# Performance work log

Hardware: AMD Instinct MI355X
Metric: run time of the kernel (lower is better)

## Reference

```python
import jax, jax.numpy as jnp
import numpy as np

LL = 1 << 20            # Fastfood padded size (power of 2 >= DD)
DD = 1024 * 768         # out_features * in_features
OUT, IN = 1024, 768


def fwht(v):
    """Unnormalized fast Walsh-Hadamard transform over a length-2^k vector."""
    n = v.shape[0]
    h = 1
    while h < n:
        v = v.reshape(-1, 2, h)
        v = jnp.concatenate([v[:, 0] + v[:, 1], v[:, 0] - v[:, 1]], axis=-1)
        h *= 2
    return v.reshape(n)


def setup_inputs() -> dict:
    key = jax.random.key(0)
    ks = jax.random.split(key, 7)
    x = jax.random.normal(ks[0], (8, 2048, IN), dtype=jnp.float32)
    theta = jax.random.normal(ks[1], (2048,), dtype=jnp.float32)
    W_0 = jax.random.normal(ks[2], (OUT, IN), dtype=jnp.float32) * 0.02
    b = jax.random.normal(ks[3], (OUT,), dtype=jnp.float32) * 0.02
    # Rademacher +/-1 diagonal
    BB = (jax.random.bernoulli(ks[4], 0.5, (LL,)).astype(jnp.float32) * 2.0 - 1.0)
    GG = jax.random.normal(ks[5], (LL,), dtype=jnp.float32)
    Pi = jax.random.permutation(ks[6], LL).astype(jnp.int64)
    return {"x": x, "theta": theta, "W_0": W_0, "b": b, "BB": BB, "GG": GG, "Pi": Pi}


def reference(x, theta, W_0, b, BB, GG, Pi):
    # pad intrinsic parameter to LL (theta.numel() < LL branch)
    theta_pad = jnp.zeros((LL,), dtype=theta.dtype).at[: theta.shape[0]].set(theta)
    # Fastfood: H B theta -> permute -> G diag -> H
    v = fwht(BB * theta_pad)
    v = v[Pi] * GG
    v = fwht(v)
    divisor = jnp.sqrt(LL * jnp.sum(GG * GG))
    update_vec = v[:DD] / (divisor * np.sqrt(float(DD) / LL))
    W_eff = W_0 + update_vec.reshape(OUT, IN)
    return jnp.einsum("bsi,oi->bso", x, W_eff) + b
```

## Files before the change

kernel.cpp:

```cpp
#include <hip/hip_runtime.h>
#include <hip/hip_bf16.h>


#define LL (1 << 20)
#define DD (1024 * 768)
#define OUTF 1024
#define INF 768
#define MROWS 16384

typedef __attribute__((ext_vector_type(8))) short s16x8;
typedef __attribute__((ext_vector_type(4))) float f32x4;
typedef __attribute__((ext_vector_type(16))) float f32x16;

__device__ __forceinline__ unsigned short f2bf(float f) {
    union { float f; unsigned u; } v; v.f = f;
    unsigned r = v.u + 0x7FFF + ((v.u >> 16) & 1);
    return (unsigned short)(r >> 16);
}

__device__ __forceinline__ unsigned cvt_pk_bf16(float lo, float hi) {
    unsigned r;
    asm("v_cvt_pk_bf16_f32 %0, %1, %2" : "=v"(r) : "v"(lo), "v"(hi));
    return r;
}

__global__ void k01_cast_r01(const float* __restrict__ X, ushort* __restrict__ XB,
                             const float* __restrict__ BB, const float* __restrict__ theta,
                             float* __restrict__ r01g) {
    __shared__ float sx[2048];
    const int t = threadIdx.x;
    if (blockIdx.x < 2048) {
        const f32x4* X4 = (const f32x4*)X;
        s16x8* O = (s16x8*)XB;
        size_t i = (size_t)blockIdx.x * 256 + t;
        #pragma unroll
        for (int j = 0; j < 3; j++, i += 524288) {
            const f32x4 A = X4[2 * i];
            const f32x4 B = X4[2 * i + 1];
            union { s16x8 v; unsigned u[4]; } o;
            o.u[0] = cvt_pk_bf16(A.x, A.y);
            o.u[1] = cvt_pk_bf16(A.z, A.w);
            o.u[2] = cvt_pk_bf16(B.x, B.y);
            o.u[3] = cvt_pk_bf16(B.z, B.w);
            O[i] = o.v;
        }
        return;
    }
    const int r = t >> 7, tt = t & 127, lane = t & 63;
    float v[8];
    {
        const float4 a0 = *(const float4*)&BB[r * 1024 + tt * 8];
        const float4 a1 = *(const float4*)&BB[r * 1024 + tt * 8 + 4];
        const float4 b0 = *(const float4*)&theta[r * 1024 + tt * 8];
        const float4 b1 = *(const float4*)&theta[r * 1024 + tt * 8 + 4];
        v[0] = a0.x * b0.x; v[1] = a0.y * b0.y; v[2] = a0.z * b0.z; v[3] = a0.w * b0.w;
        v[4] = a1.x * b1.x; v[5] = a1.y * b1.y; v[6] = a1.z * b1.z; v[7] = a1.w * b1.w;
    }
    float a;
    a = v[0]; v[0] = a + v[1]; v[1] = a - v[1];
    a = v[2]; v[2] = a + v[3]; v[3] = a - v[3];
    a = v[4]; v[4] = a + v[5]; v[5] = a - v[5];
    a = v[6]; v[6] = a + v[7]; v[7] = a - v[7];
    a = v[0]; v[0] = a + v[2]; v[2] = a - v[2];
    a = v[1]; v[1] = a + v[3]; v[3] = a - v[3];
    a = v[4]; v[4] = a + v[6]; v[6] = a - v[6];
    a = v[5]; v[5] = a + v[7]; v[7] = a - v[7];
    a = v[0]; v[0] = a + v[4]; v[4] = a - v[4];
    a = v[1]; v[1] = a + v[5]; v[5] = a - v[5];
    a = v[2]; v[2] = a + v[6]; v[6] = a - v[6];
    a = v[3]; v[3] = a + v[7]; v[7] = a - v[7];
    #pragma unroll
    for (int j = 0; j < 6; j++) {
        const float sgn = ((lane >> j) & 1) ? -1.0f : 1.0f;
        #pragma unroll
        for (int c = 0; c < 8; c++) {
            float o = __shfl_xor(v[c], 1 << j, 64);
            v[c] = fmaf(sgn, v[c], o);
        }
    }
    #pragma unroll
    for (int c = 0; c < 8; c++) sx[r * 1024 + tt * 8 + c] = v[c];
    __syncthreads();
    {
        const int pt = r * 1024 + (tt ^ 64) * 8;
        const float sgn = (tt & 64) ? -1.0f : 1.0f;
        #pragma unroll
        for (int c = 0; c < 8; c++) v[c] = fmaf(sgn, v[c], sx[pt + c]);
    }
    #pragma unroll
    for (int c = 0; c < 8; c++) r01g[r * 1024 + tt * 8 + c] = v[c];
}

__global__ __launch_bounds__(1024)
void k3_gather_fwht_lo(const int* __restrict__ Pi, const float* __restrict__ GG,
                       const float* __restrict__ r01g, f32x4* __restrict__ T2,
                       float* __restrict__ partial) {
    __shared__ float r01s[2048];
    __shared__ f32x4 sA[1024];
    __shared__ float sB[4 * 1028];
    __shared__ float ws[16];
    const int t = threadIdx.x;
    const int s_r = t >> 8, tt = t & 255, lane = t & 63;
    const int row = blockIdx.x * 4 + s_r;

    r01s[t] = r01g[t];
    r01s[t + 1024] = r01g[t + 1024];
    const int4   pv = ((const int4*)Pi)[row * 256 + tt];
    const float4 gv = ((const float4*)GG)[row * 256 + tt];
    float g2 = gv.x * gv.x + gv.y * gv.y + gv.z * gv.z + gv.w * gv.w;
    #pragma unroll
    for (int o = 32; o > 0; o >>= 1) g2 += __shfl_down(g2, o, 64);
    if (lane == 0) ws[t >> 6] = g2;
    __syncthreads();

    float v[4];
    {
        int p; float g;
        p = pv.x; g = gv.x;
        v[0] = (r01s[p & 1023] + (((p >> 10) & 1) ? -1.0f : 1.0f) * r01s[1024 + (p & 1023)]) * g;
        p = pv.y; g = gv.y;
        v[1] = (r01s[p & 1023] + (((p >> 10) & 1) ? -1.0f : 1.0f) * r01s[1024 + (p & 1023)]) * g;
        p = pv.z; g = gv.z;
        v[2] = (r01s[p & 1023] + (((p >> 10) & 1) ? -1.0f : 1.0f) * r01s[1024 + (p & 1023)]) * g;
        p = pv.w; g = gv.w;
        v[3] = (r01s[p & 1023] + (((p >> 10) & 1) ? -1.0f : 1.0f) * r01s[1024 + (p & 1023)]) * g;
    }
    float a;
    a = v[0]; v[0] = a + v[1]; v[1] = a - v[1];
    a = v[2]; v[2] = a + v[3]; v[3] = a - v[3];
    a = v[0]; v[0] = a + v[2]; v[2] = a - v[2];
    a = v[1]; v[1] = a + v[3]; v[3] = a - v[3];
    #pragma unroll
    for (int j = 0; j < 6; j++) {
        const float sgn = ((lane >> j) & 1) ? -1.0f : 1.0f;
        #pragma unroll
        for (int c = 0; c < 4; c++) {
            float o = __shfl_xor(v[c], 1 << j, 64);
            v[c] = fmaf(sgn, v[c], o);
        }
    }
    {
        f32x4 vv; vv.x = v[0]; vv.y = v[1]; vv.z = v[2]; vv.w = v[3];
        sA[t] = vv;
    }
    __syncthreads();
    {
        const int b = t & ~192;
        const f32x4 q00 = sA[b];
        const f32x4 q10 = sA[b + 64];
        const f32x4 q01 = sA[b + 128];
        const f32x4 q11 = sA[b + 192];
        const float s8 = (tt & 64) ? -1.0f : 1.0f;
        const float s9 = (tt & 128) ? -1.0f : 1.0f;
        #pragma unroll
        for (int c = 0; c < 4; c++)
            v[c] = (q00[c] + s9 * q01[c]) + s8 * (q10[c] + s9 * q11[c]);
    }
    if (t == 0) {
        float s = 0;
        #pragma unroll
        for (int i = 0; i < 16; i++) s += ws[i];
        partial[blockIdx.x] = s;
    }
    {
        f32x4 vv; vv.x = v[0]; vv.y = v[1]; vv.z = v[2]; vv.w = v[3];
        *(f32x4*)&sB[s_r * 1028 + 4 * tt] = vv;
    }
    __syncthreads();
    {
        const int rl = t & 3;
        const int lo4 = t >> 2;
        const f32x4 w = *(const f32x4*)&sB[rl * 1028 + lo4 * 4];
        T2[(size_t)lo4 * 1024 + blockIdx.x * 4 + rl] = w;
    }
}

__global__ __launch_bounds__(1024)
void k4_fwht_hi(const f32x4* __restrict__ T2, const float* __restrict__ partial,
                const float* __restrict__ W0, ushort* __restrict__ WB) {
    __shared__ f32x4 sx[1024];
    __shared__ float rw[17];
    const int t = threadIdx.x;
    const int g = blockIdx.x;
    const int lane = t & 63;

    float pr = 0.0f;
    if (t < 256) pr = partial[t];
    #pragma unroll
    for (int o = 32; o > 0; o >>= 1) pr += __shfl_down(pr, o, 64);
    if (t < 256 && lane == 0) rw[t >> 6] = pr;

    f32x4 vv = T2[(size_t)g * 1024 + t];
    #pragma unroll
    for (int j = 0; j < 6; j++) {
        const float sgn = ((lane >> j) & 1) ? -1.0f : 1.0f;
        #pragma unroll
        for (int c = 0; c < 4; c++) {
            float o = __shfl_xor(vv[c], 1 << j, 64);
            vv[c] = fmaf(sgn, vv[c], o);
        }
    }
    sx[t] = vv;
    __syncthreads();
    if (t == 0) rw[16] = rw[0] + rw[1] + rw[2] + rw[3];
    {
        const int b = t & ~192;
        const f32x4 q00 = sx[b];
        const f32x4 q10 = sx[b + 64];
        const f32x4 q01 = sx[b + 128];
        const f32x4 q11 = sx[b + 192];
        const float s6 = (t & 64) ? -1.0f : 1.0f;
        const float s7 = (t & 128) ? -1.0f : 1.0f;
        #pragma unroll
        for (int c = 0; c < 4; c++)
            vv[c] = (q00[c] + s7 * q01[c]) + s6 * (q10[c] + s7 * q11[c]);
    }
    __syncthreads();
    sx[t] = vv;
    __syncthreads();
    {
        const int b = t & ~768;
        const f32x4 q00 = sx[b];
        const f32x4 q10 = sx[b + 256];
        const f32x4 q01 = sx[b + 512];
        const f32x4 q11 = sx[b + 768];
        const float s8 = (t & 256) ? -1.0f : 1.0f;
        const float s9 = (t & 512) ? -1.0f : 1.0f;
        #pragma unroll
        for (int c = 0; c < 4; c++)
            vv[c] = (q00[c] + s9 * q01[c]) + s8 * (q10[c] + s9 * q11[c]);
    }
    if (t < 768) {
        const float scale = rsqrtf(rw[16] * (float)DD);
        const size_t d = (size_t)t * 1024 + 4 * g;
        const float4 w = *(const float4*)&W0[d];
        ushort4 o;
        o.x = f2bf(w.x + vv.x * scale);
        o.y = f2bf(w.y + vv.y * scale);
        o.z = f2bf(w.z + vv.z * scale);
        o.w = f2bf(w.w + vv.w * scale);
        *(ushort4*)&WB[d] = o;
    }
}

#define BM 128
#define BN 128
#define BK 64
#define KITERS (INF / BK)

__global__ __launch_bounds__(256)
void k7_gemm(const ushort* __restrict__ A, const ushort* __restrict__ B,
             const float* __restrict__ bias, float* __restrict__ C) {
    __shared__ ushort As[2][BM * BK];
    __shared__ ushort Bs[2][BN * BK];
    const int tid  = threadIdx.x;
    const int lane = tid & 63;
    const int wave = tid >> 6;
    const int m0 = blockIdx.x * BM;
    const int n0 = blockIdx.y * BN;
    const int wm = (wave & 1) * 64;
    const int wn = (wave >> 1) * 64;

    const int fr_row = lane & 31;
    const int fr_kh  = lane >> 5;

    f32x16 acc[2][2];
    #pragma unroll
    for (int i = 0; i < 2; i++)
        #pragma unroll
        for (int j = 0; j < 2; j++) acc[i][j] = (f32x16)(0.0f);

    auto stage = [&](int bsel, int kt) {
        #pragma unroll
        for (int i = 0; i < 4; i++) {
            const int s   = i * 256 + tid;
            const int row = s >> 3;
            const int kc  = (s & 7) ^ (row & 7);
            const ushort* ga = A + (size_t)(m0 + row) * INF + kt + kc * 8;
            const ushort* gb = B + (size_t)(n0 + row) * INF + kt + kc * 8;
            __builtin_amdgcn_global_load_lds(
                (const __attribute__((address_space(1))) void*)ga,
                (__attribute__((address_space(3))) void*)&As[bsel][i * 2048 + wave * 512], 16, 0, 0);
            __builtin_amdgcn_global_load_lds(
                (const __attribute__((address_space(1))) void*)gb,
                (__attribute__((address_space(3))) void*)&Bs[bsel][i * 2048 + wave * 512], 16, 0, 0);
        }
    };

    stage(0, 0);
    __syncthreads();

    for (int t = 0; t < KITERS; t++) {
        const int cur = t & 1;
        if (t + 1 < KITERS) stage(cur ^ 1, (t + 1) * BK);

        const ushort* Ab = As[cur];
        const ushort* Bb = Bs[cur];
        #pragma unroll
        for (int ks = 0; ks < 4; ks++) {
            const int kc = ks * 2 + fr_kh;
            s16x8 af[2], bf[2];
            #pragma unroll
            for (int mi = 0; mi < 2; mi++) {
                const int r = wm + mi * 32 + fr_row;
                af[mi] = *(const s16x8*)&Ab[(r * 8 + (kc ^ (r & 7))) * 8];
            }
            #pragma unroll
            for (int ni = 0; ni < 2; ni++) {
                const int r = wn + ni * 32 + fr_row;
                bf[ni] = *(const s16x8*)&Bb[(r * 8 + (kc ^ (r & 7))) * 8];
            }
            #pragma unroll
            for (int mi = 0; mi < 2; mi++)
                #pragma unroll
                for (int ni = 0; ni < 2; ni++)
                    acc[mi][ni] = __builtin_amdgcn_mfma_f32_32x32x16_bf16(
                        af[mi], bf[ni], acc[mi][ni], 0, 0, 0);
        }
        __syncthreads();
    }

    const int ccol = lane & 31;
    const int rbase = (lane >> 5) * 4;
    #pragma unroll
    for (int ni = 0; ni < 2; ni++) {
        const int n = n0 + wn + ni * 32 + ccol;
        const float bv = bias[n];
        #pragma unroll
        for (int mi = 0; mi < 2; mi++) {
            const int mb = m0 + wm + mi * 32 + rbase;
            #pragma unroll
            for (int r = 0; r < 16; r++) {
                const int m = mb + (r & 3) + 8 * (r >> 2);
                C[(size_t)m * OUTF + n] = acc[mi][ni][r] + bv;
            }
        }
    }
}

extern "C" void kernel_launch(void* const* d_in, const int* in_sizes, int n_in,
                              void* d_out, int out_size, void* d_ws, size_t ws_size,
                              hipStream_t stream) {
    (void)in_sizes; (void)n_in; (void)out_size; (void)ws_size;
    const float* x     = (const float*)d_in[0];
    const float* theta = (const float*)d_in[1];
    const float* W0    = (const float*)d_in[2];
    const float* bias  = (const float*)d_in[3];
    const float* BB    = (const float*)d_in[4];
    const float* GG    = (const float*)d_in[5];
    const int*   Pi    = (const int*)d_in[6];
    float* out = (float*)d_out;

    char* ws = (char*)d_ws;
    ushort* XB   = (ushort*)ws;
    f32x4*  T2   = (f32x4*)(ws + 25165824);
    ushort* WB   = (ushort*)(ws + 29360128);
    float*  R01  = (float*)(ws + 30932992);
    float*  PART = (float*)(ws + 30941184);

    k01_cast_r01    <<<2049, 256, 0, stream>>>(x, XB, BB, theta, R01);
    k3_gather_fwht_lo<<<256, 1024, 0, stream>>>(Pi, GG, R01, T2, PART);
    k4_fwht_hi      <<<256, 1024, 0, stream>>>(T2, PART, W0, WB);
    k7_gemm<<<dim3(MROWS/BM, OUTF/BN), 256, 0, stream>>>(XB, WB, bias, out);
}
```

Before: 165.1 us.

## Fuse x bf16 cast into GEMM loads and recompute theta FWHT per block

Removes the separate kernel that cast x to bf16 and computed the first 2048-point Hadamard stage. The GEMM now loads fp32 x into registers, converts it to bf16 and writes it to LDS after the MFMA loop, which avoids a 24MB write and re-read of the bf16 copy. Each gather block recomputes the small 2048-element FWHT with shuffles and LDS. The grid is also swapped so that N-tiles sharing an A row panel run adjacently. The trade-off is twice the fp32 A traffic inside the GEMM, higher register pressure, and A is no longer staged with direct-to-LDS loads.

```diff
diff --git a/kernel.cpp b/kernel.cpp
--- a/kernel.cpp
+++ b/kernel.cpp
@@ -24,77 +24,10 @@
     return r;
 }
 
-__global__ void k01_cast_r01(const float* __restrict__ X, ushort* __restrict__ XB,
-                             const float* __restrict__ BB, const float* __restrict__ theta,
-                             float* __restrict__ r01g) {
-    __shared__ float sx[2048];
-    const int t = threadIdx.x;
-    if (blockIdx.x < 2048) {
-        const f32x4* X4 = (const f32x4*)X;
-        s16x8* O = (s16x8*)XB;
-        size_t i = (size_t)blockIdx.x * 256 + t;
-        #pragma unroll
-        for (int j = 0; j < 3; j++, i += 524288) {
-            const f32x4 A = X4[2 * i];
-            const f32x4 B = X4[2 * i + 1];
-            union { s16x8 v; unsigned u[4]; } o;
-            o.u[0] = cvt_pk_bf16(A.x, A.y);
-            o.u[1] = cvt_pk_bf16(A.z, A.w);
-            o.u[2] = cvt_pk_bf16(B.x, B.y);
-            o.u[3] = cvt_pk_bf16(B.z, B.w);
-            O[i] = o.v;
-        }
-        return;
-    }
-    const int r = t >> 7, tt = t & 127, lane = t & 63;
-    float v[8];
-    {
-        const float4 a0 = *(const float4*)&BB[r * 1024 + tt * 8];
-        const float4 a1 = *(const float4*)&BB[r * 1024 + tt * 8 + 4];
-        const float4 b0 = *(const float4*)&theta[r * 1024 + tt * 8];
-        const float4 b1 = *(const float4*)&theta[r * 1024 + tt * 8 + 4];
-        v[0] = a0.x * b0.x; v[1] = a0.y * b0.y; v[2] = a0.z * b0.z; v[3] = a0.w * b0.w;
-        v[4] = a1.x * b1.x; v[5] = a1.y * b1.y; v[6] = a1.z * b1.z; v[7] = a1.w * b1.w;
-    }
-    float a;
-    a = v[0]; v[0] = a + v[1]; v[1] = a - v[1];
-    a = v[2]; v[2] = a + v[3]; v[3] = a - v[3];
-    a = v[4]; v[4] = a + v[5]; v[5] = a - v[5];
-    a = v[6]; v[6] = a + v[7]; v[7] = a - v[7];
-    a = v[0]; v[0] = a + v[2]; v[2] = a - v[2];
-    a = v[1]; v[1] = a + v[3]; v[3] = a - v[3];
-    a = v[4]; v[4] = a + v[6]; v[6] = a - v[6];
-    a = v[5]; v[5] = a + v[7]; v[7] = a - v[7];
-    a = v[0]; v[0] = a + v[4]; v[4] = a - v[4];
-    a = v[1]; v[1] = a + v[5]; v[5] = a - v[5];
-    a = v[2]; v[2] = a + v[6]; v[6] = a - v[6];
-    a = v[3]; v[3] = a + v[7]; v[7] = a - v[7];
-    #pragma unroll
-    for (int j = 0; j < 6; j++) {
-        const float sgn = ((lane >> j) & 1) ? -1.0f : 1.0f;
-        #pragma unroll
-        for (int c = 0; c < 8; c++) {
-            float o = __shfl_xor(v[c], 1 << j, 64);
-            v[c] = fmaf(sgn, v[c], o);
-        }
-    }
-    #pragma unroll
-    for (int c = 0; c < 8; c++) sx[r * 1024 + tt * 8 + c] = v[c];
-    __syncthreads();
-    {
-        const int pt = r * 1024 + (tt ^ 64) * 8;
-        const float sgn = (tt & 64) ? -1.0f : 1.0f;
-        #pragma unroll
-        for (int c = 0; c < 8; c++) v[c] = fmaf(sgn, v[c], sx[pt + c]);
-    }
-    #pragma unroll
-    for (int c = 0; c < 8; c++) r01g[r * 1024 + tt * 8 + c] = v[c];
-}
-
 __global__ __launch_bounds__(1024)
 void k3_gather_fwht_lo(const int* __restrict__ Pi, const float* __restrict__ GG,
-                       const float* __restrict__ r01g, f32x4* __restrict__ T2,
-                       float* __restrict__ partial) {
+                       const float* __restrict__ BB, const float* __restrict__ theta,
+                       f32x4* __restrict__ T2, float* __restrict__ partial) {
     __shared__ float r01s[2048];
     __shared__ f32x4 sA[1024];
     __shared__ float sB[4 * 1028];
@@ -103,14 +36,47 @@
     const int s_r = t >> 8, tt = t & 255, lane = t & 63;
     const int row = blockIdx.x * 4 + s_r;
 
-    r01s[t] = r01g[t];
-    r01s[t + 1024] = r01g[t + 1024];
     const int4   pv = ((const int4*)Pi)[row * 256 + tt];
     const float4 gv = ((const float4*)GG)[row * 256 + tt];
+
+    float w0 = BB[t] * theta[t];
+    float w1 = BB[t + 1024] * theta[t + 1024];
+    #pragma unroll
+    for (int j = 0; j < 6; j++) {
+        const float sgn = ((lane >> j) & 1) ? -1.0f : 1.0f;
+        float o0 = __shfl_xor(w0, 1 << j, 64);
+        float o1 = __shfl_xor(w1, 1 << j, 64);
+        w0 = fmaf(sgn, w0, o0);
+        w1 = fmaf(sgn, w1, o1);
+    }
+    float2* sr = (float2*)sB;
+    sr[t] = make_float2(w0, w1);
+    __syncthreads();
+    {
+        const int b = t & ~192;
+        const float2 q00 = sr[b], q10 = sr[b + 64], q01 = sr[b + 128], q11 = sr[b + 192];
+        const float s6 = (t & 64) ? -1.0f : 1.0f;
+        const float s7 = (t & 128) ? -1.0f : 1.0f;
+        w0 = (q00.x + s7 * q01.x) + s6 * (q10.x + s7 * q11.x);
+        w1 = (q00.y + s7 * q01.y) + s6 * (q10.y + s7 * q11.y);
+    }
+    __syncthreads();
+    sr[t] = make_float2(w0, w1);
     float g2 = gv.x * gv.x + gv.y * gv.y + gv.z * gv.z + gv.w * gv.w;
     #pragma unroll
     for (int o = 32; o > 0; o >>= 1) g2 += __shfl_down(g2, o, 64);
     if (lane == 0) ws[t >> 6] = g2;
+    __syncthreads();
+    {
+        const int b = t & ~768;
+        const float2 q00 = sr[b], q10 = sr[b + 256], q01 = sr[b + 512], q11 = sr[b + 768];
+        const float s8 = (t & 256) ? -1.0f : 1.0f;
+        const float s9 = (t & 512) ? -1.0f : 1.0f;
+        w0 = (q00.x + s9 * q01.x) + s8 * (q10.x + s9 * q11.x);
+        w1 = (q00.y + s9 * q01.y) + s8 * (q10.y + s9 * q11.y);
+    }
+    r01s[t] = w0;
+    r01s[1024 + t] = w1;
     __syncthreads();
 
     float v[4];
@@ -249,15 +215,15 @@
 #define KITERS (INF / BK)
 
 __global__ __launch_bounds__(256)
-void k7_gemm(const ushort* __restrict__ A, const ushort* __restrict__ B,
+void k7_gemm(const float* __restrict__ A, const ushort* __restrict__ B,
              const float* __restrict__ bias, float* __restrict__ C) {
     __shared__ ushort As[2][BM * BK];
     __shared__ ushort Bs[2][BN * BK];
     const int tid  = threadIdx.x;
     const int lane = tid & 63;
     const int wave = tid >> 6;
-    const int m0 = blockIdx.x * BM;
-    const int n0 = blockIdx.y * BN;
+    const int n0 = blockIdx.x * BN;
+    const int m0 = blockIdx.y * BM;
     const int wm = (wave & 1) * 64;
     const int wn = (wave >> 1) * 64;
 
@@ -270,29 +236,60 @@
         #pragma unroll
         for (int j = 0; j < 2; j++) acc[i][j] = (f32x16)(0.0f);
 
-    auto stage = [&](int bsel, int kt) {
+    int arow[4], akc[4];
+    #pragma unroll
+    for (int j = 0; j < 4; j++) {
+        const int s = j * 256 + tid;
+        arow[j] = s >> 3;
+        akc[j]  = (s & 7) ^ (arow[j] & 7);
+    }
+
+    f32x4 ar[8];
+    auto loadA = [&](int kt) {
+        #pragma unroll
+        for (int j = 0; j < 4; j++) {
+            const float* ga = A + (size_t)(m0 + arow[j]) * INF + kt + akc[j] * 8;
+            ar[2 * j]     = *(const f32x4*)ga;
+            ar[2 * j + 1] = *(const f32x4*)(ga + 4);
+        }
+    };
+    auto writeA = [&](int bsel) {
+        #pragma unroll
+        for (int j = 0; j < 4; j++) {
+            union { s16x8 v; unsigned u[4]; } o;
+            const f32x4 lo = ar[2 * j], hi = ar[2 * j + 1];
+            o.u[0] = cvt_pk_bf16(lo.x, lo.y);
+            o.u[1] = cvt_pk_bf16(lo.z, lo.w);
+            o.u[2] = cvt_pk_bf16(hi.x, hi.y);
+            o.u[3] = cvt_pk_bf16(hi.z, hi.w);
+            *(s16x8*)&As[bsel][(j * 256 + tid) * 8] = o.v;
+        }
+    };
+    auto stageB = [&](int bsel, int kt) {
         #pragma unroll
         for (int i = 0; i < 4; i++) {
             const int s   = i * 256 + tid;
             const int row = s >> 3;
             const int kc  = (s & 7) ^ (row & 7);
-            const ushort* ga = A + (size_t)(m0 + row) * INF + kt + kc * 8;
             const ushort* gb = B + (size_t)(n0 + row) * INF + kt + kc * 8;
-            __builtin_amdgcn_global_load_lds(
-                (const __attribute__((address_space(1))) void*)ga,
-                (__attribute__((address_space(3))) void*)&As[bsel][i * 2048 + wave * 512], 16, 0, 0);
             __builtin_amdgcn_global_load_lds(
                 (const __attribute__((address_space(1))) void*)gb,
                 (__attribute__((address_space(3))) void*)&Bs[bsel][i * 2048 + wave * 512], 16, 0, 0);
         }
     };
 
-    stage(0, 0);
+    loadA(0);
+    stageB(0, 0);
+    writeA(0);
     __syncthreads();
 
     for (int t = 0; t < KITERS; t++) {
         const int cur = t & 1;
-        if (t + 1 < KITERS) stage(cur ^ 1, (t + 1) * BK);
+        const bool pf = (t + 1 < KITERS);
+        if (pf) {
+            loadA((t + 1) * BK);
+            stageB(cur ^ 1, (t + 1) * BK);
+        }
 
         const ushort* Ab = As[cur];
         const ushort* Bb = Bs[cur];
@@ -317,6 +314,7 @@
                     acc[mi][ni] = __builtin_amdgcn_mfma_f32_32x32x16_bf16(
                         af[mi], bf[ni], acc[mi][ni], 0, 0, 0);
         }
+        if (pf) writeA(cur ^ 1);
         __syncthreads();
     }
 
@@ -352,14 +350,11 @@
     float* out = (float*)d_out;
 
     char* ws = (char*)d_ws;
-    ushort* XB   = (ushort*)ws;
-    f32x4*  T2   = (f32x4*)(ws + 25165824);
-    ushort* WB   = (ushort*)(ws + 29360128);
-    float*  R01  = (float*)(ws + 30932992);
-    float*  PART = (float*)(ws + 30941184);
-
-    k01_cast_r01    <<<2049, 256, 0, stream>>>(x, XB, BB, theta, R01);
-    k3_gather_fwht_lo<<<256, 1024, 0, stream>>>(Pi, GG, R01, T2, PART);
+    f32x4*  T2   = (f32x4*)ws;
+    ushort* WB   = (ushort*)(ws + 4194304);
+    float*  PART = (float*)(ws + 5767168);
+
+    k3_gather_fwht_lo<<<256, 1024, 0, stream>>>(Pi, GG, BB, theta, T2, PART);
     k4_fwht_hi      <<<256, 1024, 0, stream>>>(T2, PART, W0, WB);
-    k7_gemm<<<dim3(MROWS/BM, OUTF/BN), 256, 0, stream>>>(XB, WB, bias, out);
-}
+    k7_gemm<<<dim3(OUTF/BN, MROWS/BM), 256, 0, stream>>>(x, WB, bias, out);
+}
```

Result: slower. 185.8 us (+12.6%).
